# Kernel tuning notes

Measured on AMD Instinct MI355X. Metric: run time of the kernel, lower is better.

Reference implementation:

```python
import jax, jax.numpy as jnp
import numpy as np

N, D, K = 16384, 512, 512
TEMP = 0.1
EPS = 1e-8
MAX_ITERS = 100
RTOL, ATOL = 1e-4, 1e-8  # torch.allclose(rtol=1e-4)


def setup_inputs() -> dict:
    key = jax.random.key(0)
    kx, kp = jax.random.split(key)
    x = jax.random.normal(kx, (N, D), dtype=jnp.float32)
    # torch.randperm(N)[:k] -> unique initial centroid row indices
    init_idx = jax.random.permutation(kp, N)[:K].astype(jnp.int32)
    return {"x": x, "init_idx": init_idx}


def _segment_mean(x, ids, k):
    # per-cluster mean; empty clusters get a 0 centroid (torch yields NaN which is
    # later masked to 0 in the logits -- same final logits, but numerically safe)
    sums = jax.ops.segment_sum(x, ids, num_segments=k)
    cnt = jax.ops.segment_sum(jnp.ones((x.shape[0],), x.dtype), ids, num_segments=k)
    return sums / jnp.maximum(cnt, 1.0)[:, None]


def _kmeans_ids(x, init_idx):
    k = init_idx.shape[0]
    x_sq = jnp.sum(x * x, axis=1)  # [N]

    def assign(c):
        # squared euclidean distance; argmin is identical to argmin of cdist
        d2 = x_sq[:, None] + jnp.sum(c * c, axis=1)[None, :] - 2.0 * (x @ c.T)  # [N, k]
        return jnp.argmin(d2, axis=1).astype(jnp.int32)

    def cond(state):
        i, _, _, done = state
        return (i < MAX_ITERS) & (~done)

    def body(state):
        i, c, _, _ = state
        ids = assign(c)
        new_c = _segment_mean(x, ids, k)
        conv = jnp.all(jnp.abs(c - new_c) <= (ATOL + RTOL * jnp.abs(new_c)))
        c_next = jnp.where(conv, c, new_c)  # torch breaks BEFORE updating centroids
        return (i + 1, c_next, ids, conv)

    init = (jnp.int32(0), x[init_idx], jnp.zeros((x.shape[0],), jnp.int32), jnp.bool_(False))
    _, _, ids, _ = jax.lax.while_loop(cond, body, init)
    return ids


def reference(x, init_idx):
    k = init_idx.shape[0]
    ids = _kmeans_ids(x, init_idx)                 # [N] pseudo labels
    centers = _segment_mean(x, ids, k)             # [k, D]
    xn = x / (jnp.linalg.norm(x, axis=1, keepdims=True) + EPS)
    cn = centers / (jnp.linalg.norm(centers, axis=1, keepdims=True) + EPS)
    logits = (xn @ cn.T) / (TEMP + EPS)            # [N, k] cosine-sim logits
    logits = jnp.where(jnp.isnan(logits), 0.0, logits)
    logp = jax.nn.log_softmax(logits, axis=1)
    loss = -jnp.mean(jnp.take_along_axis(logp, ids[:, None], axis=1))
    return loss
```

## Files before the change

kernel.cpp:

```cpp
#include <hip/hip_runtime.h>

#define NPTS 16384
#define DIM 512
#define KCL 512
#define TEMPV 0.1f
#define EPSV 1e-8f
#define MAXIT 100
#define RTOLV 1e-4f
#define ATOLV 1e-8f
#define NSLC 8

typedef float f32x4 __attribute__((ext_vector_type(4)));
typedef short s16x8 __attribute__((ext_vector_type(8)));


__device__ inline float blockReduceSum256(float v) {
    #pragma unroll
    for (int o = 32; o > 0; o >>= 1) v += __shfl_down(v, o, 64);
    __shared__ float wsum[4];
    int lane = threadIdx.x & 63, w = threadIdx.x >> 6;
    if (lane == 0) wsum[w] = v;
    __syncthreads();
    float r = 0.f;
    if (threadIdx.x == 0) r = wsum[0] + wsum[1] + wsum[2] + wsum[3];
    return r;
}

__device__ inline unsigned short bf16rne(float v) {
    unsigned u = __float_as_uint(v);
    return (unsigned short)((u + 0x7FFFu + ((u >> 16) & 1u)) >> 16);
}

__device__ inline bool iterDead(const unsigned* done, const unsigned* viol, int it) {
    if (*done) return true;
    if (it > 0 && viol[(it - 1) & 1] == 0u) return true;
    return false;
}


__global__ __launch_bounds__(256) void k_init0(const float* __restrict__ x,
                                               const int* __restrict__ idx,
                                               float* __restrict__ c, float* __restrict__ ct,
                                               unsigned short* __restrict__ ch,
                                               unsigned long long* __restrict__ packed,
                                               unsigned* __restrict__ counts,
                                               unsigned* __restrict__ done,
                                               unsigned* __restrict__ viol,
                                               float* __restrict__ loss, int do_split) {
    int e = blockIdx.x * 256 + threadIdx.x;
    int j = e >> 9, d = e & 511;
    float v = x[(size_t)idx[j] * DIM + d];
    c[e] = v;
    ct[(size_t)d * KCL + j] = v;
    if (do_split) ch[e] = bf16rne(v);
    if (e < NPTS) packed[e] = ~0ull;
    if (e < KCL) counts[e] = 0u;
    if (e == 0) { *done = 0u; viol[0] = 0u; viol[1] = 0u; *loss = 0.f; }
}

__global__ __launch_bounds__(256) void k_csq0(const float* __restrict__ c, float* __restrict__ c_sq) {
    int j = blockIdx.x, t = threadIdx.x;
    float a = c[(size_t)j * DIM + t], b = c[(size_t)j * DIM + t + 256];
    float s = blockReduceSum256(a * a + b * b);
    if (t == 0) c_sq[j] = s;
}

__global__ __launch_bounds__(256) void k_splitx(const float* __restrict__ x,
                                                unsigned short* __restrict__ xh) {
    int e4 = blockIdx.x * 256 + threadIdx.x;
    float4 v = reinterpret_cast<const float4*>(x)[e4];
    ushort4 h;
    h.x = bf16rne(v.x); h.y = bf16rne(v.y); h.z = bf16rne(v.z); h.w = bf16rne(v.w);
    reinterpret_cast<ushort4*>(xh)[e4] = h;
}


__global__ __launch_bounds__(256) void k_assign_mfma(
        const unsigned short* __restrict__ xh,
        const unsigned short* __restrict__ ch,
        const float* __restrict__ csq,
        unsigned long long* __restrict__ packed,
        unsigned* __restrict__ viol,
        unsigned* __restrict__ done, int it) {
    bool lead = (blockIdx.x == 0 && blockIdx.y == 0 && threadIdx.x == 0);
    if (*done) return;
    if (it > 0 && viol[(it - 1) & 1] == 0u) {
        if (lead) *done = 1u;
        return;
    }
    if (lead) viol[it & 1] = 0u;

    __shared__ unsigned short Bs[32768];

    int tid = threadIdx.x;
    int w = tid >> 6, l = tid & 63;
    int lr = l & 15, lg = l >> 4;
    int row0 = blockIdx.y * 256 + w * 64;
    int col0 = blockIdx.x * 128;

    f32x4 acc[4][8];
    #pragma unroll
    for (int rf = 0; rf < 4; ++rf)
        #pragma unroll
        for (int cf = 0; cf < 8; ++cf) acc[rf][cf] = (f32x4){0.f, 0.f, 0.f, 0.f};

    const unsigned short* ap = xh + (size_t)(row0 + lr) * DIM + 8 * lg;

    #pragma unroll
    for (int s = 0; s < 2; ++s) {
        {
            int f = tid;
            #pragma unroll
            for (int i = 0; i < 16; ++i, f += 256) {
                int col = f >> 5, kg = f & 31;
                s16x8 v = *(const s16x8*)(ch + (size_t)(col0 + col) * DIM + s * 256 + kg * 8);
                int slot = col * 32 + (kg ^ (col & 7));
                *(s16x8*)&Bs[slot * 8] = v;
            }
        }
        __syncthreads();
        #pragma unroll
        for (int kk = 0; kk < 8; ++kk) {
            int kbase = s * 256 + kk * 32;
            s16x8 a[4];
            #pragma unroll
            for (int rf = 0; rf < 4; ++rf)
                a[rf] = *(const s16x8*)(ap + kbase + (size_t)rf * 16 * DIM);
            #pragma unroll
            for (int cf = 0; cf < 8; ++cf) {
                int col = cf * 16 + lr;
                int slot = col * 32 + ((kk * 4 + lg) ^ (lr & 7));
                s16x8 b = *(const s16x8*)&Bs[slot * 8];
                #pragma unroll
                for (int rf = 0; rf < 4; ++rf)
                    acc[rf][cf] = __builtin_amdgcn_mfma_f32_16x16x32_bf16(a[rf], b, acc[rf][cf], 0, 0, 0);
            }
        }
        __syncthreads();
    }

    float cs[8];
    #pragma unroll
    for (int cf = 0; cf < 8; ++cf) cs[cf] = csq[col0 + cf * 16 + lr];

    #pragma unroll
    for (int rf = 0; rf < 4; ++rf) {
        #pragma unroll
        for (int r = 0; r < 4; ++r) {
            float best = 3.0e38f; int bj = 0;
            #pragma unroll
            for (int cf = 0; cf < 8; ++cf) {
                float v = cs[cf] - 2.0f * acc[rf][cf][r];
                if (v < best) { best = v; bj = col0 + cf * 16 + lr; }
            }
            unsigned u = __float_as_uint(best);
            u ^= ((int)u < 0) ? 0xFFFFFFFFu : 0x80000000u;
            unsigned long long key = ((unsigned long long)u << 32) | (unsigned)bj;
            #pragma unroll
            for (int m = 1; m <= 8; m <<= 1) {
                unsigned long long o = __shfl_xor(key, m, 64);
                key = (o < key) ? o : key;
            }
            if (lr == 0) atomicMin(&packed[row0 + rf * 16 + lg * 4 + r], key);
        }
    }
}


__global__ __launch_bounds__(256) void k_gather(
        const unsigned long long* __restrict__ packed,
        const unsigned short* __restrict__ xh,
        float* __restrict__ gsum, unsigned* __restrict__ gcnt,
        const unsigned* __restrict__ viol, const unsigned* __restrict__ done, int it) {
    if (iterDead(done, viol, it)) return;
    int j = blockIdx.x, s = blockIdx.y, t = threadIdx.x;
    const unsigned* pid = (const unsigned*)packed;
    const unsigned* xr32 = (const unsigned*)xh;
    __shared__ int list[256];
    __shared__ int lcnt;
    float a0 = 0.f, a1 = 0.f;
    int cnt = 0;
    int base0 = s * (NPTS / NSLC);
    for (int chunk = 0; chunk < (NPTS / NSLC) / 256; ++chunk) {
        if (t == 0) lcnt = 0;
        __syncthreads();
        int i = base0 + chunk * 256 + t;
        int ji = (int)pid[2 * i];
        if (ji == j) { int p = atomicAdd(&lcnt, 1); list[p] = i; }
        __syncthreads();
        int n = lcnt;
        for (int p = 0; p < n; ++p) {
            unsigned u = xr32[(size_t)list[p] * 256 + t];
            a0 += __uint_as_float(u << 16);
            a1 += __uint_as_float(u & 0xffff0000u);
        }
        cnt += n;
        __syncthreads();
    }
    float2* dst = (float2*)(gsum + ((size_t)s * KCL + j) * DIM);
    dst[t] = make_float2(a0, a1);
    if (t == 0) gcnt[s * KCL + j] = (unsigned)cnt;
}


__global__ __launch_bounds__(256) void k_update(
        float* __restrict__ c,
        const float* __restrict__ gsum, const unsigned* __restrict__ gcnt,
        float* __restrict__ c_sq, unsigned short* __restrict__ ch,
        unsigned long long* __restrict__ packed, int* __restrict__ ids,
        unsigned* __restrict__ viol, const unsigned* __restrict__ done, int it) {
    if (iterDead(done, viol, it)) return;
    int j = blockIdx.x, t = threadIdx.x;
    float a0 = 0.f, a1 = 0.f;
    unsigned cnt = 0;
    #pragma unroll
    for (int s = 0; s < NSLC; ++s) {
        float2 v = ((const float2*)(gsum + ((size_t)s * KCL + j) * DIM))[t];
        a0 += v.x; a1 += v.y;
        cnt += gcnt[s * KCL + j];
    }
    float cf = fmaxf((float)cnt, 1.f);
    float n0 = a0 / cf, n1 = a1 / cf;
    float2 cc = ((const float2*)(c + (size_t)j * DIM))[t];
    bool bad = !((fabsf(cc.x - n0) <= ATOLV + RTOLV * fabsf(n0)) &&
                 (fabsf(cc.y - n1) <= ATOLV + RTOLV * fabsf(n1)));
    unsigned long long bm = __ballot(bad);
    if ((t & 63) == 0 && bm) atomicOr(&viol[it & 1], 1u);
    ((float2*)(c + (size_t)j * DIM))[t] = make_float2(n0, n1);
    ((unsigned*)(ch + (size_t)j * DIM))[t] =
        (unsigned)bf16rne(n0) | ((unsigned)bf16rne(n1) << 16);
    float ss = blockReduceSum256(n0 * n0 + n1 * n1);
    if (t == 0) c_sq[j] = ss;
    if (t < 32) {
        int i = j * 32 + t;
        ids[i] = (int)(unsigned)(packed[i] & 0xffffffffull);
        packed[i] = ~0ull;
    }
}


__global__ __launch_bounds__(256) void k_invx(const float* __restrict__ x, float* __restrict__ invx) {
    int r = blockIdx.x, t = threadIdx.x;
    float a = x[(size_t)r * DIM + t], b = x[(size_t)r * DIM + t + 256];
    float s = blockReduceSum256(a * a + b * b);
    if (t == 0) invx[r] = 1.f / ((sqrtf(s) + EPSV) * (TEMPV + EPSV));
}

__global__ __launch_bounds__(256) void k_cn(const float* __restrict__ src, float* __restrict__ cn,
                                            unsigned short* __restrict__ cnh, int do_split) {
    int j = blockIdx.x, t = threadIdx.x;
    float a = src[(size_t)j * DIM + t], b = src[(size_t)j * DIM + t + 256];
    float s = blockReduceSum256(a * a + b * b);
    __shared__ float bc;
    if (t == 0) bc = 1.f / (sqrtf(s) + EPSV);
    __syncthreads();
    float v0 = a * bc, v1 = b * bc;
    cn[(size_t)j * DIM + t] = v0;
    cn[(size_t)j * DIM + t + 256] = v1;
    if (do_split) {
        cnh[(size_t)j * DIM + t] = bf16rne(v0);
        cnh[(size_t)j * DIM + t + 256] = bf16rne(v1);
    }
}

__global__ __launch_bounds__(256) void k_logits_mfma(
        const unsigned short* __restrict__ xh,
        const unsigned short* __restrict__ cnh,
        const float* __restrict__ invx,
        float* __restrict__ pmax, float* __restrict__ psum) {
    int tid = threadIdx.x;
    int w = tid >> 6, l = tid & 63;
    int lr = l & 15, lg = l >> 4;
    int row0 = blockIdx.y * 128 + w * 32;
    int col0 = blockIdx.x * 128;
    int jb = blockIdx.x;

    f32x4 acc[2][8];
    #pragma unroll
    for (int rf = 0; rf < 2; ++rf)
        #pragma unroll
        for (int cf = 0; cf < 8; ++cf) acc[rf][cf] = (f32x4){0.f, 0.f, 0.f, 0.f};

    const unsigned short* a0p = xh + (size_t)(row0 + lr) * DIM + 8 * lg;
    const unsigned short* a1p = a0p + (size_t)16 * DIM;
    const unsigned short* bp  = cnh + (size_t)(col0 + lr) * DIM + 8 * lg;

    #pragma unroll 2
    for (int k0 = 0; k0 < DIM; k0 += 32) {
        s16x8 a0 = *reinterpret_cast<const s16x8*>(a0p + k0);
        s16x8 a1 = *reinterpret_cast<const s16x8*>(a1p + k0);
        #pragma unroll
        for (int cf = 0; cf < 8; ++cf) {
            s16x8 b = *reinterpret_cast<const s16x8*>(bp + (size_t)cf * 16 * DIM + k0);
            acc[0][cf] = __builtin_amdgcn_mfma_f32_16x16x32_bf16(a0, b, acc[0][cf], 0, 0, 0);
            acc[1][cf] = __builtin_amdgcn_mfma_f32_16x16x32_bf16(a1, b, acc[1][cf], 0, 0, 0);
        }
    }

    #pragma unroll
    for (int rf = 0; rf < 2; ++rf) {
        #pragma unroll
        for (int r = 0; r < 4; ++r) {
            int row = row0 + rf * 16 + lg * 4 + r;
            float inv = invx[row];
            float m = -3.0e38f;
            #pragma unroll
            for (int cf = 0; cf < 8; ++cf) m = fmaxf(m, acc[rf][cf][r] * inv);
            #pragma unroll
            for (int msk = 1; msk <= 8; msk <<= 1) m = fmaxf(m, __shfl_xor(m, msk, 64));
            float s = 0.f;
            #pragma unroll
            for (int cf = 0; cf < 8; ++cf) s += expf(acc[rf][cf][r] * inv - m);
            #pragma unroll
            for (int msk = 1; msk <= 8; msk <<= 1) s += __shfl_xor(s, msk, 64);
            if (lr == 0) {
                pmax[(size_t)row * 4 + jb] = m;
                psum[(size_t)row * 4 + jb] = s;
            }
        }
    }
}

__global__ __launch_bounds__(256) void k_loss(const float* __restrict__ x,
                                              const float* __restrict__ cn,
                                              const int* __restrict__ ids,
                                              const float* __restrict__ invx,
                                              const float* __restrict__ pmax,
                                              const float* __restrict__ psum,
                                              float* __restrict__ loss) {
    int i = blockIdx.x * 256 + threadIdx.x;
    float M = -1e30f;
    #pragma unroll
    for (int b = 0; b < 4; ++b) M = fmaxf(M, pmax[(size_t)i * 4 + b]);
    float S = 0.f;
    #pragma unroll
    for (int b = 0; b < 4; ++b) S += psum[(size_t)i * 4 + b] * expf(pmax[(size_t)i * 4 + b] - M);
    float lse = M + logf(S);
    int j = ids[i];
    const float4* xr = (const float4*)(x + (size_t)i * DIM);
    const float4* cr = (const float4*)(cn + (size_t)j * DIM);
    float dot = 0.f;
    for (int q = 0; q < 128; ++q) {
        float4 a = xr[q], b = cr[q];
        dot += a.x * b.x + a.y * b.y + a.z * b.z + a.w * b.w;
    }
    float t = dot * invx[i];
    float contrib = lse - t;
    float s = blockReduceSum256(contrib);
    if (threadIdx.x == 0) atomicAdd(loss, s);
}

__global__ void k_final(const float* __restrict__ loss, float* __restrict__ out) {
    out[0] = *loss / (float)NPTS;
}


__global__ __launch_bounds__(256) void k_assign(const float* __restrict__ x,
                                                const float* __restrict__ ct,
                                                const float* __restrict__ csq,
                                                unsigned long long* __restrict__ packed,
                                                const unsigned* __restrict__ done) {
    if (*done) return;
    __shared__ float As[16][128];
    __shared__ float Bs[16][128];
    __shared__ float redv[128][17];
    __shared__ int   redj[128][17];

    int tid = threadIdx.x;
    int ty = tid >> 4, tx = tid & 15;
    int row0 = blockIdx.x * 128, col0 = blockIdx.y * 128;

    float acc[8][8];
    #pragma unroll
    for (int i = 0; i < 8; ++i)
        #pragma unroll
        for (int j = 0; j < 8; ++j) acc[i][j] = 0.f;

    for (int dk = 0; dk < DIM; dk += 16) {
        {
            int r = tid >> 1;
            int d0 = (tid & 1) * 8;
            const float4* src = reinterpret_cast<const float4*>(&x[(size_t)(row0 + r) * DIM + dk + d0]);
            float4 v0 = src[0], v1 = src[1];
            As[d0 + 0][r] = v0.x; As[d0 + 1][r] = v0.y; As[d0 + 2][r] = v0.z; As[d0 + 3][r] = v0.w;
            As[d0 + 4][r] = v1.x; As[d0 + 5][r] = v1.y; As[d0 + 6][r] = v1.z; As[d0 + 7][r] = v1.w;
        }
        {
            int d = tid >> 4;
            int c0 = (tid & 15) * 8;
            const float4* src = reinterpret_cast<const float4*>(&ct[(size_t)(dk + d) * KCL + col0 + c0]);
            float4 v0 = src[0], v1 = src[1];
            *reinterpret_cast<float4*>(&Bs[d][c0]) = v0;
            *reinterpret_cast<float4*>(&Bs[d][c0 + 4]) = v1;
        }
        __syncthreads();
        #pragma unroll
        for (int kk = 0; kk < 16; ++kk) {
            float a[8], b[8];
            *(float4*)&a[0] = *(const float4*)&As[kk][ty * 8];
            *(float4*)&a[4] = *(const float4*)&As[kk][ty * 8 + 4];
            *(float4*)&b[0] = *(const float4*)&Bs[kk][tx * 8];
            *(float4*)&b[4] = *(const float4*)&Bs[kk][tx * 8 + 4];
            #pragma unroll
            for (int i = 0; i < 8; ++i)
                #pragma unroll
                for (int j = 0; j < 8; ++j) acc[i][j] = fmaf(a[i], b[j], acc[i][j]);
        }
        __syncthreads();
    }

    #pragma unroll
    for (int i = 0; i < 8; ++i) {
        float best = 1e30f; int bj = col0 + tx * 8;
        #pragma unroll
        for (int j = 0; j < 8; ++j) {
            int col = col0 + tx * 8 + j;
            float v = csq[col] - 2.f * acc[i][j];
            if (v < best) { best = v; bj = col; }
        }
        redv[ty * 8 + i][tx] = best;
        redj[ty * 8 + i][tx] = bj;
    }
    __syncthreads();
    if (tid < 128) {
        float best = 1e30f; int bj = 0x7fffffff;
        for (int t2 = 0; t2 < 16; ++t2) {
            float v = redv[tid][t2]; int j = redj[tid][t2];
            if (v < best || (v == best && j < bj)) { best = v; bj = j; }
        }
        unsigned u = __float_as_uint(best);
        u ^= (u >> 31) ? 0xFFFFFFFFu : 0x80000000u;
        unsigned long long key = ((unsigned long long)u << 32) | (unsigned)bj;
        atomicMin(&packed[row0 + tid], key);
    }
}

__global__ __launch_bounds__(256) void k_hist(const unsigned long long* __restrict__ packed,
                                              int* __restrict__ ids, unsigned* __restrict__ counts,
                                              const unsigned* __restrict__ done) {
    if (*done) return;
    int i = blockIdx.x * 256 + threadIdx.x;
    unsigned long long p = packed[i];
    int j = (int)(unsigned)(p & 0xffffffffull);
    ids[i] = j;
    atomicAdd(&counts[j], 1u);
}

__global__ void k_scan(const unsigned* __restrict__ counts, unsigned* __restrict__ offsets,
                       unsigned* __restrict__ cursors, const unsigned* __restrict__ done) {
    if (*done) return;
    __shared__ unsigned s[512];
    int t = threadIdx.x;
    unsigned c0 = counts[t];
    s[t] = c0;
    __syncthreads();
    for (int off = 1; off < 512; off <<= 1) {
        unsigned v = (t >= off) ? s[t - off] : 0u;
        __syncthreads();
        s[t] += v;
        __syncthreads();
    }
    unsigned excl = s[t] - c0;
    offsets[t] = excl;
    cursors[t] = excl;
}

__global__ __launch_bounds__(256) void k_scatter(const int* __restrict__ ids,
                                                 unsigned* __restrict__ cursors,
                                                 int* __restrict__ order,
                                                 const unsigned* __restrict__ done) {
    if (*done) return;
    int i = blockIdx.x * 256 + threadIdx.x;
    int j = ids[i];
    unsigned pos = atomicAdd(&cursors[j], 1u);
    order[pos] = i;
}

__global__ __launch_bounds__(256) void k_sumconv(const float* __restrict__ x,
                                                 const int* __restrict__ order,
                                                 const unsigned* __restrict__ offsets,
                                                 const unsigned* __restrict__ counts,
                                                 const float* __restrict__ c,
                                                 float* __restrict__ new_c,
                                                 unsigned* __restrict__ viol,
                                                 const unsigned* __restrict__ done, int it) {
    if (*done) return;
    int j = blockIdx.x, t = threadIdx.x;
    unsigned cnt = counts[j], base = offsets[j];
    float a0 = 0.f, a1 = 0.f;
    for (unsigned p = 0; p < cnt; ++p) {
        int i = order[base + p];
        const float* xr = x + (size_t)i * DIM;
        a0 += xr[t]; a1 += xr[t + 256];
    }
    float cf = fmaxf((float)cnt, 1.f);
    float n0 = a0 / cf, n1 = a1 / cf;
    new_c[(size_t)j * DIM + t] = n0;
    new_c[(size_t)j * DIM + t + 256] = n1;
    float c0 = c[(size_t)j * DIM + t], c1 = c[(size_t)j * DIM + t + 256];
    bool ok = (fabsf(c0 - n0) <= ATOLV + RTOLV * fabsf(n0)) &&
              (fabsf(c1 - n1) <= ATOLV + RTOLV * fabsf(n1));
    unsigned long long bad = __ballot(!ok);
    if ((t & 63) == 0 && bad) atomicOr(&viol[it & 1], 1u);
}

__global__ __launch_bounds__(256) void k_commit(float* __restrict__ c, const float* __restrict__ new_c,
                                                float* __restrict__ c_sq,
                                                unsigned long long* __restrict__ packed,
                                                unsigned* __restrict__ counts,
                                                unsigned* __restrict__ viol,
                                                unsigned* __restrict__ done, int it) {
    if (*done) return;
    unsigned v = viol[it & 1];
    int b = blockIdx.x, t = threadIdx.x;
    int e = b * 256 + t;
    if (v) {
        float n0 = new_c[(size_t)b * DIM + t], n1 = new_c[(size_t)b * DIM + t + 256];
        c[(size_t)b * DIM + t] = n0;
        c[(size_t)b * DIM + t + 256] = n1;
        float s = blockReduceSum256(n0 * n0 + n1 * n1);
        if (t == 0) c_sq[b] = s;
    } else {
        if (e == 0) *done = 1u;
    }
    if (e < NPTS) packed[e] = ~0ull;
    if (e < KCL) counts[e] = 0u;
    if (e == 0) viol[(it + 1) & 1] = 0u;
}

__global__ void k_trans(const float* __restrict__ src, float* __restrict__ dst,
                        const unsigned* __restrict__ done, int check) {
    if (check && *done) return;
    __shared__ float tile[32][33];
    int bx = blockIdx.x & 15, by = blockIdx.x >> 4;
    int tx = threadIdx.x & 31, ty = threadIdx.x >> 5;
    #pragma unroll
    for (int q = 0; q < 4; ++q) {
        int r = by * 32 + ty + q * 8;
        tile[ty + q * 8][tx] = src[(size_t)r * DIM + bx * 32 + tx];
    }
    __syncthreads();
    #pragma unroll
    for (int q = 0; q < 4; ++q) {
        int d = bx * 32 + ty + q * 8;
        dst[(size_t)d * KCL + by * 32 + tx] = tile[tx][ty + q * 8];
    }
}

__global__ __launch_bounds__(256) void k_logits(const float* __restrict__ x,
                                                const float* __restrict__ ct,
                                                const float* __restrict__ invx,
                                                float* __restrict__ pmax, float* __restrict__ psum) {
    __shared__ float As[16][128];
    __shared__ float Bs[16][128];
    __shared__ float red2[128][17];
    __shared__ float rowm[128];

    int tid = threadIdx.x;
    int ty = tid >> 4, tx = tid & 15;
    int row0 = blockIdx.x * 128, col0 = blockIdx.y * 128;
    int jb = blockIdx.y;

    float acc[8][8];
    #pragma unroll
    for (int i = 0; i < 8; ++i)
        #pragma unroll
        for (int j = 0; j < 8; ++j) acc[i][j] = 0.f;

    for (int dk = 0; dk < DIM; dk += 16) {
        {
            int r = tid >> 1;
            int d0 = (tid & 1) * 8;
            const float4* src = reinterpret_cast<const float4*>(&x[(size_t)(row0 + r) * DIM + dk + d0]);
            float4 v0 = src[0], v1 = src[1];
            As[d0 + 0][r] = v0.x; As[d0 + 1][r] = v0.y; As[d0 + 2][r] = v0.z; As[d0 + 3][r] = v0.w;
            As[d0 + 4][r] = v1.x; As[d0 + 5][r] = v1.y; As[d0 + 6][r] = v1.z; As[d0 + 7][r] = v1.w;
        }
        {
            int d = tid >> 4;
            int c0 = (tid & 15) * 8;
            const float4* src = reinterpret_cast<const float4*>(&ct[(size_t)(dk + d) * KCL + col0 + c0]);
            float4 v0 = src[0], v1 = src[1];
            *reinterpret_cast<float4*>(&Bs[d][c0]) = v0;
            *reinterpret_cast<float4*>(&Bs[d][c0 + 4]) = v1;
        }
        __syncthreads();
        #pragma unroll
        for (int kk = 0; kk < 16; ++kk) {
            float a[8], b[8];
            *(float4*)&a[0] = *(const float4*)&As[kk][ty * 8];
            *(float4*)&a[4] = *(const float4*)&As[kk][ty * 8 + 4];
            *(float4*)&b[0] = *(const float4*)&Bs[kk][tx * 8];
            *(float4*)&b[4] = *(const float4*)&Bs[kk][tx * 8 + 4];
            #pragma unroll
            for (int i = 0; i < 8; ++i)
                #pragma unroll
                for (int j = 0; j < 8; ++j) acc[i][j] = fmaf(a[i], b[j], acc[i][j]);
        }
        __syncthreads();
    }

    float inv[8];
    #pragma unroll
    for (int i = 0; i < 8; ++i) inv[i] = invx[row0 + ty * 8 + i];

    #pragma unroll
    for (int i = 0; i < 8; ++i) {
        float m = -1e30f;
        #pragma unroll
        for (int j = 0; j < 8; ++j) m = fmaxf(m, acc[i][j] * inv[i]);
        red2[ty * 8 + i][tx] = m;
    }
    __syncthreads();
    if (tid < 128) {
        float m = -1e30f;
        for (int t2 = 0; t2 < 16; ++t2) m = fmaxf(m, red2[tid][t2]);
        rowm[tid] = m;
    }
    __syncthreads();
    #pragma unroll
    for (int i = 0; i < 8; ++i) {
        float M = rowm[ty * 8 + i];
        float s = 0.f;
        #pragma unroll
        for (int j = 0; j < 8; ++j) s += expf(acc[i][j] * inv[i] - M);
        red2[ty * 8 + i][tx] = s;
    }
    __syncthreads();
    if (tid < 128) {
        float s = 0.f;
        for (int t2 = 0; t2 < 16; ++t2) s += red2[tid][t2];
        pmax[(size_t)(row0 + tid) * 4 + jb] = rowm[tid];
        psum[(size_t)(row0 + tid) * 4 + jb] = s;
    }
}


extern "C" void kernel_launch(void* const* d_in, const int* in_sizes, int n_in,
                              void* d_out, int out_size, void* d_ws, size_t ws_size,
                              hipStream_t stream) {
    const float* x = (const float*)d_in[0];
    const int* init_idx = (const int*)d_in[1];
    float* out = (float*)d_out;

    char* w = (char*)d_ws;
    float* c      = (float*)w; w += (size_t)KCL * DIM * 4;
    float* new_c  = (float*)w; w += (size_t)KCL * DIM * 4;
    float* ct     = (float*)w; w += (size_t)DIM * KCL * 4;
    float* c_sq   = (float*)w; w += KCL * 4;
    unsigned* counts  = (unsigned*)w; w += KCL * 4;
    unsigned* offsets = (unsigned*)w; w += KCL * 4;
    unsigned* cursors = (unsigned*)w; w += KCL * 4;
    unsigned* done = (unsigned*)w; w += 64;
    unsigned* viol = (unsigned*)w; w += 64;
    float* loss    = (float*)w; w += 64;
    int* ids   = (int*)w; w += NPTS * 4;
    int* order = (int*)w; w += NPTS * 4;
    unsigned long long* packed = (unsigned long long*)w; w += NPTS * 8;
    float* invx = (float*)w; w += NPTS * 4;
    float* pmax = (float*)w; w += (size_t)NPTS * 4 * 4;
    float* psum = (float*)w; w += (size_t)NPTS * 4 * 4;
    unsigned short* ch = (unsigned short*)w; w += (size_t)KCL * DIM * 2;
    unsigned short* cnh = (unsigned short*)w; w += (size_t)KCL * DIM * 2;
    unsigned short* xh = (unsigned short*)w; w += (size_t)NPTS * DIM * 2;
    float* gsum = (float*)w; w += (size_t)NSLC * KCL * DIM * 4;
    unsigned* gcnt = (unsigned*)w; w += (size_t)NSLC * KCL * 4;
    size_t need = (size_t)(w - (char*)d_ws);
    int use_mfma = (ws_size >= need) ? 1 : 0;

    k_init0<<<1024, 256, 0, stream>>>(x, init_idx, c, ct, ch, packed, counts, done, viol, loss, use_mfma);
    k_csq0<<<KCL, 256, 0, stream>>>(c, c_sq);
    if (use_mfma)
        k_splitx<<<NPTS * DIM / 4 / 256, 256, 0, stream>>>(x, xh);

    for (int it = 0; it < MAXIT; ++it) {
        if (use_mfma) {
            k_assign_mfma<<<dim3(4, 64), 256, 0, stream>>>(xh, ch, c_sq, packed, viol, done, it);
            k_gather<<<dim3(KCL, NSLC), 256, 0, stream>>>(packed, xh, gsum, gcnt, viol, done, it);
            k_update<<<KCL, 256, 0, stream>>>(c, gsum, gcnt, c_sq, ch, packed, ids, viol, done, it);
        } else {
            k_assign<<<dim3(128, 4), 256, 0, stream>>>(x, ct, c_sq, packed, done);
            k_hist<<<64, 256, 0, stream>>>(packed, ids, counts, done);
            k_scan<<<1, 512, 0, stream>>>(counts, offsets, cursors, done);
            k_scatter<<<64, 256, 0, stream>>>(ids, cursors, order, done);
            k_sumconv<<<KCL, 256, 0, stream>>>(x, order, offsets, counts, c, new_c, viol, done, it);
            k_commit<<<KCL, 256, 0, stream>>>(c, new_c, c_sq, packed, counts, viol, done, it);
            k_trans<<<256, 256, 0, stream>>>(new_c, ct, done, 1);
        }
    }

    k_invx<<<NPTS, 256, 0, stream>>>(x, invx);
    if (use_mfma) {
        k_cn<<<KCL, 256, 0, stream>>>(c, c, cnh, 1);
        k_logits_mfma<<<dim3(4, 128), 256, 0, stream>>>(xh, cnh, invx, pmax, psum);
    } else {
        k_cn<<<KCL, 256, 0, stream>>>(new_c, c, cnh, 0);
        k_trans<<<256, 256, 0, stream>>>(c, ct, done, 0);
        k_logits<<<dim3(128, 4), 256, 0, stream>>>(x, ct, invx, pmax, psum);
    }
    k_loss<<<64, 256, 0, stream>>>(x, c, ids, invx, pmax, psum, loss);
    k_final<<<1, 1, 0, stream>>>(loss, out);
}
```

Before: 1.358 ms.

## Fuse gather and centroid update into one kernel with ping-pong assignment buffers

Merges the per-slice gather kernel and the update kernel into a single kernel, one block per cluster, that scans all points and then computes the new centroid, the convergence check, the bf16 copy and the squared norm. Assignment keys are double-buffered so the fused kernel can reset the next iteration's buffer while other blocks still read the current one. This removes one launch per iteration and the partial-sum buffers, and each block prefetches the next chunk of packed ids. In exchange, parallelism drops from 4096 to 512 blocks, so each block scans all 16384 ids serially.

Measured after the change: 1.711 ms. 26.0% more time.

```diff
diff --git a/kernel.cpp b/kernel.cpp
--- a/kernel.cpp
+++ b/kernel.cpp
@@ -42,7 +42,8 @@
                                                const int* __restrict__ idx,
                                                float* __restrict__ c, float* __restrict__ ct,
                                                unsigned short* __restrict__ ch,
-                                               unsigned long long* __restrict__ packed,
+                                               unsigned long long* __restrict__ packed0,
+                                               unsigned long long* __restrict__ packed1,
                                                unsigned* __restrict__ counts,
                                                unsigned* __restrict__ done,
                                                unsigned* __restrict__ viol,
@@ -53,7 +54,7 @@
     c[e] = v;
     ct[(size_t)d * KCL + j] = v;
     if (do_split) ch[e] = bf16rne(v);
-    if (e < NPTS) packed[e] = ~0ull;
+    if (e < NPTS) { packed0[e] = ~0ull; packed1[e] = ~0ull; }
     if (e < KCL) counts[e] = 0u;
     if (e == 0) { *done = 0u; viol[0] = 0u; viol[1] = 0u; *loss = 0.f; }
 }
@@ -167,26 +168,32 @@
 }
 
 
-__global__ __launch_bounds__(256) void k_gather(
+__global__ __launch_bounds__(256) void k_gatherupd(
         const unsigned long long* __restrict__ packed,
+        unsigned long long* __restrict__ packed_next,
         const unsigned short* __restrict__ xh,
-        float* __restrict__ gsum, unsigned* __restrict__ gcnt,
-        const unsigned* __restrict__ viol, const unsigned* __restrict__ done, int it) {
+        float* __restrict__ c, float* __restrict__ c_sq,
+        unsigned short* __restrict__ ch, int* __restrict__ ids,
+        unsigned* __restrict__ viol, const unsigned* __restrict__ done, int it) {
     if (iterDead(done, viol, it)) return;
-    int j = blockIdx.x, s = blockIdx.y, t = threadIdx.x;
-    const unsigned* pid = (const unsigned*)packed;
+    int j = blockIdx.x, t = threadIdx.x;
+    const uint4* pk4 = (const uint4*)packed;
     const unsigned* xr32 = (const unsigned*)xh;
-    __shared__ int list[256];
+
+    __shared__ int list[512];
     __shared__ int lcnt;
+
     float a0 = 0.f, a1 = 0.f;
     int cnt = 0;
-    int base0 = s * (NPTS / NSLC);
-    for (int chunk = 0; chunk < (NPTS / NSLC) / 256; ++chunk) {
+    uint4 cur = pk4[t];
+    for (int chn = 0; chn < 32; ++chn) {
+        uint4 nxt;
+        if (chn < 31) nxt = pk4[(chn + 1) * 256 + t];
         if (t == 0) lcnt = 0;
         __syncthreads();
-        int i = base0 + chunk * 256 + t;
-        int ji = (int)pid[2 * i];
-        if (ji == j) { int p = atomicAdd(&lcnt, 1); list[p] = i; }
+        int i0 = chn * 512 + 2 * t;
+        if (cur.x == (unsigned)j) list[atomicAdd(&lcnt, 1)] = i0;
+        if (cur.z == (unsigned)j) list[atomicAdd(&lcnt, 1)] = i0 + 1;
         __syncthreads();
         int n = lcnt;
         for (int p = 0; p < n; ++p) {
@@ -195,30 +202,9 @@
             a1 += __uint_as_float(u & 0xffff0000u);
         }
         cnt += n;
-        __syncthreads();
-    }
-    float2* dst = (float2*)(gsum + ((size_t)s * KCL + j) * DIM);
-    dst[t] = make_float2(a0, a1);
-    if (t == 0) gcnt[s * KCL + j] = (unsigned)cnt;
-}
-
-
-__global__ __launch_bounds__(256) void k_update(
-        float* __restrict__ c,
-        const float* __restrict__ gsum, const unsigned* __restrict__ gcnt,
-        float* __restrict__ c_sq, unsigned short* __restrict__ ch,
-        unsigned long long* __restrict__ packed, int* __restrict__ ids,
-        unsigned* __restrict__ viol, const unsigned* __restrict__ done, int it) {
-    if (iterDead(done, viol, it)) return;
-    int j = blockIdx.x, t = threadIdx.x;
-    float a0 = 0.f, a1 = 0.f;
-    unsigned cnt = 0;
-    #pragma unroll
-    for (int s = 0; s < NSLC; ++s) {
-        float2 v = ((const float2*)(gsum + ((size_t)s * KCL + j) * DIM))[t];
-        a0 += v.x; a1 += v.y;
-        cnt += gcnt[s * KCL + j];
-    }
+        cur = nxt;
+    }
+
     float cf = fmaxf((float)cnt, 1.f);
     float n0 = a0 / cf, n1 = a1 / cf;
     float2 cc = ((const float2*)(c + (size_t)j * DIM))[t];
@@ -234,7 +220,7 @@
     if (t < 32) {
         int i = j * 32 + t;
         ids[i] = (int)(unsigned)(packed[i] & 0xffffffffull);
-        packed[i] = ~0ull;
+        packed_next[i] = ~0ull;
     }
 }
 
@@ -656,35 +642,37 @@
     float* loss    = (float*)w; w += 64;
     int* ids   = (int*)w; w += NPTS * 4;
     int* order = (int*)w; w += NPTS * 4;
-    unsigned long long* packed = (unsigned long long*)w; w += NPTS * 8;
+    unsigned long long* packed0 = (unsigned long long*)w; w += NPTS * 8;
+    unsigned long long* packed1 = (unsigned long long*)w; w += NPTS * 8;
     float* invx = (float*)w; w += NPTS * 4;
     float* pmax = (float*)w; w += (size_t)NPTS * 4 * 4;
     float* psum = (float*)w; w += (size_t)NPTS * 4 * 4;
     unsigned short* ch = (unsigned short*)w; w += (size_t)KCL * DIM * 2;
     unsigned short* cnh = (unsigned short*)w; w += (size_t)KCL * DIM * 2;
     unsigned short* xh = (unsigned short*)w; w += (size_t)NPTS * DIM * 2;
-    float* gsum = (float*)w; w += (size_t)NSLC * KCL * DIM * 4;
-    unsigned* gcnt = (unsigned*)w; w += (size_t)NSLC * KCL * 4;
     size_t need = (size_t)(w - (char*)d_ws);
     int use_mfma = (ws_size >= need) ? 1 : 0;
 
-    k_init0<<<1024, 256, 0, stream>>>(x, init_idx, c, ct, ch, packed, counts, done, viol, loss, use_mfma);
+    k_init0<<<1024, 256, 0, stream>>>(x, init_idx, c, ct, ch, packed0,
+                                      use_mfma ? packed1 : packed0,
+                                      counts, done, viol, loss, use_mfma);
     k_csq0<<<KCL, 256, 0, stream>>>(c, c_sq);
     if (use_mfma)
         k_splitx<<<NPTS * DIM / 4 / 256, 256, 0, stream>>>(x, xh);
 
     for (int it = 0; it < MAXIT; ++it) {
         if (use_mfma) {
-            k_assign_mfma<<<dim3(4, 64), 256, 0, stream>>>(xh, ch, c_sq, packed, viol, done, it);
-            k_gather<<<dim3(KCL, NSLC), 256, 0, stream>>>(packed, xh, gsum, gcnt, viol, done, it);
-            k_update<<<KCL, 256, 0, stream>>>(c, gsum, gcnt, c_sq, ch, packed, ids, viol, done, it);
+            unsigned long long* pc = (it & 1) ? packed1 : packed0;
+            unsigned long long* pn = (it & 1) ? packed0 : packed1;
+            k_assign_mfma<<<dim3(4, 64), 256, 0, stream>>>(xh, ch, c_sq, pc, viol, done, it);
+            k_gatherupd<<<KCL, 256, 0, stream>>>(pc, pn, xh, c, c_sq, ch, ids, viol, done, it);
         } else {
-            k_assign<<<dim3(128, 4), 256, 0, stream>>>(x, ct, c_sq, packed, done);
-            k_hist<<<64, 256, 0, stream>>>(packed, ids, counts, done);
+            k_assign<<<dim3(128, 4), 256, 0, stream>>>(x, ct, c_sq, packed0, done);
+            k_hist<<<64, 256, 0, stream>>>(packed0, ids, counts, done);
             k_scan<<<1, 512, 0, stream>>>(counts, offsets, cursors, done);
             k_scatter<<<64, 256, 0, stream>>>(ids, cursors, order, done);
             k_sumconv<<<KCL, 256, 0, stream>>>(x, order, offsets, counts, c, new_c, viol, done, it);
-            k_commit<<<KCL, 256, 0, stream>>>(c, new_c, c_sq, packed, counts, viol, done, it);
+            k_commit<<<KCL, 256, 0, stream>>>(c, new_c, c_sq, packed0, counts, viol, done, it);
             k_trans<<<256, 256, 0, stream>>>(new_c, ct, done, 1);
         }
     }
```
